# Optimization experiments

Hardware: AMD Instinct MI355X
Metric: run time of the kernel (lower is better)

## Reference

```python
import jax, jax.numpy as jnp
import numpy as np
import math

N_HEADS = 8
TANH_CLIP = 10.0
TEMP = 1.0


def setup_inputs() -> dict:
    key = jax.random.key(0)
    ks = jax.random.split(key, 8)
    B, N, D = 256, 2048, 128
    node_embeddings = jax.random.normal(ks[0], (B, N, D), dtype=jnp.float32)
    W_node = jax.random.normal(ks[1], (D, 3 * D), dtype=jnp.float32) / math.sqrt(D)
    W_fixed = jax.random.normal(ks[2], (D, D), dtype=jnp.float32) / math.sqrt(D)
    W_step = jax.random.normal(ks[3], (2 * D, D), dtype=jnp.float32) / math.sqrt(2 * D)
    W_out = jax.random.normal(ks[4], (D, D), dtype=jnp.float32) / math.sqrt(D)
    first_idx = jax.random.randint(ks[5], (B,), 0, N, dtype=jnp.int32)
    last_idx = jax.random.randint(ks[6], (B,), 0, N, dtype=jnp.int32)
    mask = jax.random.bernoulli(ks[7], 0.5, (B, N))
    mask = mask.at[:, 0].set(False)  # guarantee at least one feasible node per row
    return {"node_embeddings": node_embeddings, "W_node": W_node, "W_fixed": W_fixed,
            "W_step": W_step, "W_out": W_out, "first_idx": first_idx,
            "last_idx": last_idx, "mask": mask}


def reference(node_embeddings, W_node, W_fixed, W_step, W_out, first_idx, last_idx, mask):
    B, N, D = node_embeddings.shape
    H = N_HEADS
    hd = D // H  # key_dim = val_dim = embed_dim / n_heads
    neg_inf = -jnp.inf

    # --- _precompute ---
    graph_embed = node_embeddings.mean(axis=1)                # [B, D]
    fixed_context = graph_embed @ W_fixed                     # [B, D]
    proj = node_embeddings @ W_node                           # [B, N, 3D]
    gK, gV, logit_K = jnp.split(proj, 3, axis=-1)             # each [B, N, D]
    gK = gK.reshape(B, N, H, hd).transpose(2, 0, 1, 3)        # [H, B, N, hd]
    gV = gV.reshape(B, N, H, hd).transpose(2, 0, 1, 3)        # [H, B, N, hd]

    # --- step context: cat(first node emb, last node emb) ---
    first_emb = jnp.take_along_axis(node_embeddings, first_idx[:, None, None].astype(jnp.int32), axis=1)[:, 0]  # [B, D]
    last_emb = jnp.take_along_axis(node_embeddings, last_idx[:, None, None].astype(jnp.int32), axis=1)[:, 0]
    step_ctx = jnp.concatenate([first_emb, last_emb], axis=-1)  # [B, 2D]
    query = fixed_context + step_ctx @ W_step                 # [B, D]

    # --- glimpse multi-head attention (n_query = 1, masked inner) ---
    Q = query.reshape(B, H, hd).transpose(1, 0, 2)            # [H, B, hd]
    compat = jnp.einsum('hbd,hbnd->hbn', Q, gK) / math.sqrt(hd)  # [H, B, N]
    compat = jnp.where(mask[None, :, :], neg_inf, compat)     # mask_inner=True
    attn = jax.nn.softmax(compat, axis=-1)
    heads = jnp.einsum('hbn,hbnd->hbd', attn, gV)             # [H, B, hd]
    glimpse = heads.transpose(1, 0, 2).reshape(B, D) @ W_out  # project_out, [B, D]

    # --- logits with tanh clipping and masking ---
    logits = jnp.einsum('bd,bnd->bn', glimpse, logit_K) / math.sqrt(D)  # [B, N]
    logits = jnp.tanh(logits) * TANH_CLIP
    logits = jnp.where(mask, neg_inf, logits)                 # mask_logits=True
    log_p = jax.nn.log_softmax(logits / TEMP, axis=-1)        # [B, N]
    return log_p
```

## Files before the change

### kernel.cpp

```cpp
#include <hip/hip_runtime.h>
#include <math.h>

#define B_ 256
#define N_ 2048
#define D_ 128

#define NEG_HUGE (-1.0e30f)

#define WSA_STRIDE 1040
#define WSA_SIZE (B_ * 8 * WSA_STRIDE)
#define WSB_OFF WSA_SIZE
#define WSB_SIZE (B_ * 8 * 2)
#define WSC_OFF (WSB_OFF + WSB_SIZE)
#define WSC_SIZE (B_ * D_)
#define WS_FLOATS (WSC_OFF + WSC_SIZE)

__device__ __forceinline__ float wave_max64(float v) {
#pragma unroll
  for (int off = 32; off > 0; off >>= 1) v = fmaxf(v, __shfl_xor(v, off, 64));
  return v;
}
__device__ __forceinline__ float wave_sum64(float v) {
#pragma unroll
  for (int off = 32; off > 0; off >>= 1) v += __shfl_xor(v, off, 64);
  return v;
}

__global__ void __launch_bounds__(128) k_partial(const float* __restrict__ emb,
                                                 float* __restrict__ buf) {
  const int b = blockIdx.x, s = blockIdx.y;
  const int t = threadIdx.x;
  const int f4 = t & 31, ng = t >> 5;
  const float4* base = (const float4*)(emb + (size_t)b * N_ * D_);
  float4 acc = make_float4(0.f, 0.f, 0.f, 0.f);
  int n = s * 256 + ng;
#pragma unroll 4
  for (int i = 0; i < 64; ++i, n += 4) {
    float4 v = base[(size_t)n * 32 + f4];
    acc.x += v.x; acc.y += v.y; acc.z += v.z; acc.w += v.w;
  }
  __shared__ float4 red[128];
  red[t] = acc;
  __syncthreads();
  if (ng == 0) {
    float4 a = red[f4], bb = red[32 + f4], c = red[64 + f4], d = red[96 + f4];
    float4 r = make_float4(a.x + bb.x + c.x + d.x, a.y + bb.y + c.y + d.y,
                           a.z + bb.z + c.z + d.z, a.w + bb.w + c.w + d.w);
    *((float4*)(buf + (size_t)b * N_ + s * 128) + f4) = r;
  }
}

__global__ void __launch_bounds__(128) k_query(const float* __restrict__ emb,
                                               const float* __restrict__ Wfix,
                                               const float* __restrict__ Wstep,
                                               const float* __restrict__ Wnode,
                                               const int* __restrict__ fidx,
                                               const int* __restrict__ lidx,
                                               float* __restrict__ buf) {
  const int b = blockIdx.x, t = threadIdx.x;
  __shared__ float ge[128], fe[128], le[128], q[128];
  float s = 0.f;
  const float* part = buf + (size_t)b * N_;
#pragma unroll
  for (int i = 0; i < 8; ++i) s += part[i * 128 + t];
  ge[t] = s * (1.0f / 2048.0f);
  const int fi = fidx[b], li = lidx[b];
  fe[t] = emb[(size_t)b * N_ * D_ + (size_t)fi * D_ + t];
  le[t] = emb[(size_t)b * N_ * D_ + (size_t)li * D_ + t];
  __syncthreads();
  float acc = 0.f;
  for (int k = 0; k < 128; ++k) acc = fmaf(ge[k], Wfix[k * 128 + t], acc);
  for (int k = 0; k < 128; ++k) acc = fmaf(fe[k], Wstep[k * 128 + t], acc);
  for (int k = 0; k < 128; ++k) acc = fmaf(le[k], Wstep[(128 + k) * 128 + t], acc);
  q[t] = acc;
  __syncthreads();
  const float* wrow = Wnode + (size_t)t * 384;
#pragma unroll
  for (int h = 0; h < 8; ++h) {
    float a = 0.f;
#pragma unroll
    for (int k = 0; k < 16; ++k) a = fmaf(q[h * 16 + k], wrow[h * 16 + k], a);
    buf[(size_t)b * N_ + 1024 + h * 128 + t] = a * 0.25f;
  }
}

__global__ void __launch_bounds__(256) k_attn_part(const float* __restrict__ emb,
                                                   const unsigned char* __restrict__ mask,
                                                   const float* __restrict__ buf,
                                                   float* __restrict__ wsA) {
  const int b = blockIdx.x, s = blockIdx.y;
  const int t = threadIdx.x;
  const int lane = t & 63;
  const int hb = t >> 6;
  const int h0 = hb, h1 = hb + 4;

  __shared__ __align__(16) float emb_lds[64][132];
  __shared__ __align__(16) float qh_s[8 * 128];
  __shared__ unsigned char mask_s[64];

  {
    const float* src = buf + (size_t)b * N_ + 1024;
    for (int i = t; i < 1024; i += 256) qh_s[i] = src[i];
  }

  float m0 = -INFINITY, m1 = -INFINITY, l0 = 0.f, l1 = 0.f;
  float w00 = 0.f, w01 = 0.f, w10 = 0.f, w11 = 0.f;
  const int d0 = lane, d1 = lane + 64;
  const float* embb = emb + (size_t)b * N_ * D_;
  const unsigned char* mrow = mask + (size_t)b * N_;

  __syncthreads();

  for (int tile = 0; tile < 4; ++tile) {
    const int n0 = s * 256 + tile * 64;
    {
      int gid = t;
#pragma unroll
      for (int i = 0; i < 8; ++i, gid += 256) {
        int r = gid >> 5, c4 = gid & 31;
        float4 v = *(const float4*)(embb + (size_t)(n0 + r) * D_ + c4 * 4);
        *(float4*)&emb_lds[r][c4 * 4] = v;
      }
      if (t < 64) mask_s[t] = mrow[n0 + t];
    }
    __syncthreads();

    float s0 = 0.f, s1 = 0.f;
    {
      const float* er = &emb_lds[lane][0];
      const float* q0r = &qh_s[h0 * 128];
      const float* q1r = &qh_s[h1 * 128];
#pragma unroll 8
      for (int k = 0; k < 32; ++k) {
        float4 e = *(const float4*)(er + 4 * k);
        float4 qa = *(const float4*)(q0r + 4 * k);
        float4 qb = *(const float4*)(q1r + 4 * k);
        s0 = fmaf(e.x, qa.x, fmaf(e.y, qa.y, fmaf(e.z, qa.z, fmaf(e.w, qa.w, s0))));
        s1 = fmaf(e.x, qb.x, fmaf(e.y, qb.y, fmaf(e.z, qb.z, fmaf(e.w, qb.w, s1))));
      }
    }
    const bool msk = mask_s[lane] != 0;
    if (msk) { s0 = -INFINITY; s1 = -INFINITY; }

    const float tm0 = wave_max64(s0), tm1 = wave_max64(s1);
    const float mn0 = fmaxf(m0, tm0), mn1 = fmaxf(m1, tm1);
    const float r0 = (mn0 == -INFINITY) ? 1.f : expf(m0 - mn0);
    const float r1 = (mn1 == -INFINITY) ? 1.f : expf(m1 - mn1);
    const float p0 = msk ? 0.f : expf(s0 - mn0);
    const float p1 = msk ? 0.f : expf(s1 - mn1);
    l0 = l0 * r0 + wave_sum64(p0);
    l1 = l1 * r1 + wave_sum64(p1);
    m0 = mn0; m1 = mn1;

    w00 *= r0; w01 *= r0; w10 *= r1; w11 *= r1;
#pragma unroll 4
    for (int n = 0; n < 64; ++n) {
      const float pa = __int_as_float(__builtin_amdgcn_readlane(__float_as_int(p0), n));
      const float pb = __int_as_float(__builtin_amdgcn_readlane(__float_as_int(p1), n));
      const float e0 = emb_lds[n][d0];
      const float e1 = emb_lds[n][d1];
      w00 = fmaf(pa, e0, w00); w01 = fmaf(pa, e1, w01);
      w10 = fmaf(pb, e0, w10); w11 = fmaf(pb, e1, w11);
    }
    __syncthreads();
  }

  float* dst = wsA + (size_t)(b * 8 + s) * WSA_STRIDE;
  dst[16 + h0 * 128 + d0] = w00;
  dst[16 + h0 * 128 + d1] = w01;
  dst[16 + h1 * 128 + d0] = w10;
  dst[16 + h1 * 128 + d1] = w11;
  if (lane == 0) {
    dst[h0] = m0; dst[8 + h0] = l0;
    dst[h1] = m1; dst[8 + h1] = l1;
  }
}

__global__ void __launch_bounds__(128) k_attn_comb(const float* __restrict__ Wnode,
                                                   const float* __restrict__ Wout,
                                                   const float* __restrict__ wsA,
                                                   float* __restrict__ wsC) {
  const int b = blockIdx.x, t = threadIdx.x;
  const float* base = wsA + (size_t)b * 8 * WSA_STRIDE;
  __shared__ float Ls[8], scale[8][8];
  __shared__ float wl[8 * 128], heads[128], glim[128];

  if (t < 8) {
    float M = -INFINITY;
#pragma unroll
    for (int s = 0; s < 8; ++s) M = fmaxf(M, base[s * WSA_STRIDE + t]);
    float L = 0.f;
#pragma unroll
    for (int s = 0; s < 8; ++s) {
      const float m = base[s * WSA_STRIDE + t];
      const float sc = (m == -INFINITY) ? 0.f : expf(m - M);
      scale[s][t] = sc;
      L = fmaf(base[s * WSA_STRIDE + 8 + t], sc, L);
    }
    Ls[t] = L;
  }
  __syncthreads();

#pragma unroll
  for (int h = 0; h < 8; ++h) {
    float acc = 0.f;
#pragma unroll
    for (int s = 0; s < 8; ++s)
      acc = fmaf(scale[s][h], base[s * WSA_STRIDE + 16 + h * 128 + t], acc);
    wl[h * 128 + t] = acc;
  }
  __syncthreads();

  {
    const int h = t >> 4, k = t & 15;
    float hv = 0.f;
    const float* wp = Wnode + 128 + h * 16 + k;
    for (int d = 0; d < 128; ++d) hv = fmaf(wl[h * 128 + d], wp[(size_t)d * 384], hv);
    heads[t] = hv / Ls[h];
  }
  __syncthreads();
  {
    float g = 0.f;
    for (int j = 0; j < 128; ++j) g = fmaf(heads[j], Wout[j * 128 + t], g);
    glim[t] = g;
  }
  __syncthreads();
  {
    float cv = 0.f;
    const float* wr = Wnode + (size_t)t * 384 + 256;
    for (int j = 0; j < 128; ++j) cv = fmaf(wr[j], glim[j], cv);
    wsC[(size_t)b * 128 + t] = cv * 0.08838834764831845f;
  }
}

__global__ void __launch_bounds__(256) k_logits_part(const float* __restrict__ emb,
                                                     const unsigned char* __restrict__ mask,
                                                     const float* __restrict__ wsC,
                                                     float* __restrict__ buf,
                                                     float* __restrict__ wsB) {
  const int b = blockIdx.x, s = blockIdx.y;
  const int t = threadIdx.x, lane = t & 63, w = t >> 6;
  __shared__ __align__(16) float emb_lds[64][132];
  __shared__ float part[4][64];
  const float* embb = emb + (size_t)b * N_ * D_;
  const unsigned char* mrow = mask + (size_t)b * N_;

  float4 cq[8];
  {
    const float4* c4 = (const float4*)(wsC + (size_t)b * 128);
#pragma unroll
    for (int j = 0; j < 8; ++j) cq[j] = c4[w * 8 + j];
  }

  float mr = NEG_HUGE, sr = 0.f;
  for (int tile = 0; tile < 4; ++tile) {
    const int n0 = s * 256 + tile * 64;
    {
      int gid = t;
#pragma unroll
      for (int i = 0; i < 8; ++i, gid += 256) {
        int r = gid >> 5, c4i = gid & 31;
        *(float4*)&emb_lds[r][c4i * 4] =
            *(const float4*)(embb + (size_t)(n0 + r) * D_ + c4i * 4);
      }
    }
    __syncthreads();

    const float* er = &emb_lds[lane][w * 32];
    float acc = 0.f;
#pragma unroll
    for (int j = 0; j < 8; ++j) {
      float4 e = *(const float4*)(er + 4 * j);
      acc = fmaf(e.x, cq[j].x, fmaf(e.y, cq[j].y, fmaf(e.z, cq[j].z, fmaf(e.w, cq[j].w, acc))));
    }
    part[w][lane] = acc;
    __syncthreads();

    const float v = part[0][lane] + part[1][lane] + part[2][lane] + part[3][lane];
    const bool msk = mrow[n0 + lane] != 0;
    const float val = msk ? NEG_HUGE : 10.f * tanhf(v);
    const float tm = wave_max64(val);
    const float mn = fmaxf(mr, tm);
    sr = sr * expf(mr - mn) + wave_sum64(msk ? 0.f : expf(val - mn));
    mr = mn;
    if (w == 0) buf[(size_t)b * N_ + n0 + lane] = val;
    __syncthreads();
  }
  if (t == 0) {
    wsB[(size_t)(b * 8 + s) * 2] = mr;
    wsB[(size_t)(b * 8 + s) * 2 + 1] = sr;
  }
}

__global__ void __launch_bounds__(256) k_norm(const float* __restrict__ wsB,
                                              float* __restrict__ buf) {
  const int b = blockIdx.x, t = threadIdx.x;
  __shared__ float LSs;
  if (t == 0) {
    float M = NEG_HUGE;
#pragma unroll
    for (int s = 0; s < 8; ++s) M = fmaxf(M, wsB[(size_t)(b * 8 + s) * 2]);
    float S = 0.f;
#pragma unroll
    for (int s = 0; s < 8; ++s) {
      const float m = wsB[(size_t)(b * 8 + s) * 2];
      S += wsB[(size_t)(b * 8 + s) * 2 + 1] * expf(m - M);
    }
    LSs = M + logf(S);
  }
  __syncthreads();
  const float LS = LSs;
#pragma unroll
  for (int i = 0; i < 8; ++i) {
    const size_t idx = (size_t)b * N_ + t + 256 * i;
    const float v = buf[idx];
    buf[idx] = (v <= -1.0e29f) ? NEG_HUGE : (v - LS);
  }
}

__global__ void __launch_bounds__(256) k_attn(const float* __restrict__ emb,
                                              const float* __restrict__ Wnode,
                                              const float* __restrict__ Wout,
                                              const unsigned char* __restrict__ mask,
                                              float* __restrict__ buf) {
  const int b = blockIdx.x;
  const int t = threadIdx.x;
  const int lane = t & 63;
  const int hb = t >> 6;
  const int h0 = hb, h1 = hb + 4;

  __shared__ __align__(16) float emb_lds[64][132];
  __shared__ __align__(16) float qh_s[8 * 128];
  __shared__ float heads_lds[128];
  __shared__ float glim_lds[128];
  __shared__ float l_lds[8];
  __shared__ unsigned char mask_s[64];

  {
    const float* src = buf + (size_t)b * N_ + 1024;
    for (int i = t; i < 1024; i += 256) qh_s[i] = src[i];
  }
  float m0 = -INFINITY, m1 = -INFINITY, l0 = 0.f, l1 = 0.f;
  float w00 = 0.f, w01 = 0.f, w10 = 0.f, w11 = 0.f;
  const int d0 = lane, d1 = lane + 64;
  const float* embb = emb + (size_t)b * N_ * D_;
  const unsigned char* mrow = mask + (size_t)b * N_;
  __syncthreads();
  for (int tile = 0; tile < N_ / 64; ++tile) {
    const int n0 = tile * 64;
    int gid = t;
#pragma unroll
    for (int i = 0; i < 8; ++i, gid += 256) {
      int r = gid >> 5, c4 = gid & 31;
      *(float4*)&emb_lds[r][c4 * 4] = *(const float4*)(embb + (size_t)(n0 + r) * D_ + c4 * 4);
    }
    if (t < 64) mask_s[t] = mrow[n0 + t];
    __syncthreads();
    float s0 = 0.f, s1 = 0.f;
    const float* er = &emb_lds[lane][0];
    const float* q0r = &qh_s[h0 * 128];
    const float* q1r = &qh_s[h1 * 128];
#pragma unroll 8
    for (int k = 0; k < 32; ++k) {
      float4 e = *(const float4*)(er + 4 * k);
      float4 qa = *(const float4*)(q0r + 4 * k);
      float4 qb = *(const float4*)(q1r + 4 * k);
      s0 = fmaf(e.x, qa.x, fmaf(e.y, qa.y, fmaf(e.z, qa.z, fmaf(e.w, qa.w, s0))));
      s1 = fmaf(e.x, qb.x, fmaf(e.y, qb.y, fmaf(e.z, qb.z, fmaf(e.w, qb.w, s1))));
    }
    const bool msk = mask_s[lane] != 0;
    if (msk) { s0 = -INFINITY; s1 = -INFINITY; }
    const float tm0 = wave_max64(s0), tm1 = wave_max64(s1);
    const float mn0 = fmaxf(m0, tm0), mn1 = fmaxf(m1, tm1);
    const float r0 = (mn0 == -INFINITY) ? 1.f : expf(m0 - mn0);
    const float r1 = (mn1 == -INFINITY) ? 1.f : expf(m1 - mn1);
    const float p0 = msk ? 0.f : expf(s0 - mn0);
    const float p1 = msk ? 0.f : expf(s1 - mn1);
    l0 = l0 * r0 + wave_sum64(p0);
    l1 = l1 * r1 + wave_sum64(p1);
    m0 = mn0; m1 = mn1;
    w00 *= r0; w01 *= r0; w10 *= r1; w11 *= r1;
#pragma unroll 4
    for (int n = 0; n < 64; ++n) {
      const float pa = __int_as_float(__builtin_amdgcn_readlane(__float_as_int(p0), n));
      const float pb = __int_as_float(__builtin_amdgcn_readlane(__float_as_int(p1), n));
      const float e0 = emb_lds[n][d0];
      const float e1 = emb_lds[n][d1];
      w00 = fmaf(pa, e0, w00); w01 = fmaf(pa, e1, w01);
      w10 = fmaf(pb, e0, w10); w11 = fmaf(pb, e1, w11);
    }
    __syncthreads();
  }
  float* wl = &emb_lds[0][0];
  wl[h0 * 128 + d0] = w00; wl[h0 * 128 + d1] = w01;
  wl[h1 * 128 + d0] = w10; wl[h1 * 128 + d1] = w11;
  if (lane == 0) { l_lds[h0] = l0; l_lds[h1] = l1; }
  __syncthreads();
  if (t < 128) {
    const int h = t >> 4, k = t & 15;
    float hv = 0.f;
    const float* wp = Wnode + 128 + h * 16 + k;
    for (int d = 0; d < 128; ++d) hv = fmaf(wl[h * 128 + d], wp[(size_t)d * 384], hv);
    heads_lds[h * 16 + k] = hv / l_lds[h];
  }
  __syncthreads();
  if (t < 128) {
    float g = 0.f;
    for (int j = 0; j < 128; ++j) g = fmaf(heads_lds[j], Wout[j * 128 + t], g);
    glim_lds[t] = g;
  }
  __syncthreads();
  if (t < 128) {
    float cv = 0.f;
    const float* wr = Wnode + (size_t)t * 384 + 256;
    for (int j = 0; j < 128; ++j) cv = fmaf(wr[j], glim_lds[j], cv);
    buf[(size_t)b * N_ + t] = cv * 0.08838834764831845f;
  }
}

__global__ void __launch_bounds__(256) k_logits(const float* __restrict__ emb,
                                                const unsigned char* __restrict__ mask,
                                                float* __restrict__ buf) {
  const int b = blockIdx.x, t = threadIdx.x;
  const int lane = t & 63, w = t >> 6;
  __shared__ float lg[N_];
  __shared__ float redmax[4], redsum[4];
  const float c0 = buf[(size_t)b * N_ + 2 * lane];
  const float c1 = buf[(size_t)b * N_ + 2 * lane + 1];
  const float2* ebase = (const float2*)(emb + (size_t)b * N_ * D_);
  for (int i = 0; i < 64; ++i) {
    const int n0 = w * 512 + i * 8;
    float sarr[8];
#pragma unroll
    for (int j = 0; j < 8; ++j) {
      float2 e = ebase[(size_t)(n0 + j) * 64 + lane];
      sarr[j] = fmaf(e.x, c0, e.y * c1);
    }
#pragma unroll
    for (int j = 0; j < 8; ++j) {
      const float v = wave_sum64(sarr[j]);
      if (lane == j) lg[n0 + j] = v;
    }
  }
  __syncthreads();
  const unsigned char* mrow = mask + (size_t)b * N_;
  float v[8];
  float vmax = NEG_HUGE;
#pragma unroll
  for (int i = 0; i < 8; ++i) {
    const int n = t + 256 * i;
    const float val = mrow[n] ? NEG_HUGE : 10.f * tanhf(lg[n]);
    v[i] = val;
    vmax = fmaxf(vmax, val);
  }
  vmax = wave_max64(vmax);
  if (lane == 0) redmax[w] = vmax;
  __syncthreads();
  const float M = fmaxf(fmaxf(redmax[0], redmax[1]), fmaxf(redmax[2], redmax[3]));
  float ss = 0.f;
#pragma unroll
  for (int i = 0; i < 8; ++i) ss += expf(v[i] - M);
  ss = wave_sum64(ss);
  if (lane == 0) redsum[w] = ss;
  __syncthreads();
  const float S = redsum[0] + redsum[1] + redsum[2] + redsum[3];
  const float LS = M + logf(S);
#pragma unroll
  for (int i = 0; i < 8; ++i) {
    const int n = t + 256 * i;
    buf[(size_t)b * N_ + n] = mrow[n] ? NEG_HUGE : (v[i] - LS);
  }
}

extern "C" void kernel_launch(void* const* d_in, const int* in_sizes, int n_in,
                              void* d_out, int out_size, void* d_ws, size_t ws_size,
                              hipStream_t stream) {
  (void)in_sizes; (void)n_in; (void)out_size;
  const float* emb = (const float*)d_in[0];
  const float* Wnode = (const float*)d_in[1];
  const float* Wfix = (const float*)d_in[2];
  const float* Wstep = (const float*)d_in[3];
  const float* Wout = (const float*)d_in[4];
  const int* fidx = (const int*)d_in[5];
  const int* lidx = (const int*)d_in[6];
  const unsigned char* mask = (const unsigned char*)d_in[7];
  float* buf = (float*)d_out;

  k_partial<<<dim3(B_, 8), 128, 0, stream>>>(emb, buf);
  k_query<<<B_, 128, 0, stream>>>(emb, Wfix, Wstep, Wnode, fidx, lidx, buf);

  if (ws_size >= (size_t)WS_FLOATS * sizeof(float)) {
    float* ws = (float*)d_ws;
    k_attn_part<<<dim3(B_, 8), 256, 0, stream>>>(emb, mask, buf, ws);
    k_attn_comb<<<B_, 128, 0, stream>>>(Wnode, Wout, ws, ws + WSC_OFF);
    k_logits_part<<<dim3(B_, 8), 256, 0, stream>>>(emb, mask, ws + WSC_OFF, buf, ws + WSB_OFF);
    k_norm<<<B_, 256, 0, stream>>>(ws + WSB_OFF, buf);
  } else {
    k_attn<<<B_, 256, 0, stream>>>(emb, Wnode, Wout, mask, buf);
    k_logits<<<B_, 256, 0, stream>>>(emb, mask, buf);
  }
}
```

Before: 199.8 us.

## Stage embeddings as bf16 copy and fuse query and combine into attention/logit kernels

A new prep kernel reads the fp32 embeddings once. It computes the per-slice mean partials and writes a bf16 (round-to-nearest-even) copy of the embeddings into workspace. The attention and logit kernels then stream this half-size copy instead of the fp32 tensor. The query projection is folded into the attention-partial kernel and the head combine/projection into the logit-partial kernel, cutting the launch count from six to four. In exchange, the small matvecs are recomputed redundantly in each of the 8 slice blocks, the path needs a large workspace, and the bf16 keys and values add numerical error.

```diff
diff --git a/kernel.cpp b/kernel.cpp
--- a/kernel.cpp
+++ b/kernel.cpp
@@ -7,13 +7,20 @@
 
 #define NEG_HUGE (-1.0e30f)
 
+#define WSE_USHORTS ((size_t)B_ * N_ * D_)
+#define WSE_BYTES (WSE_USHORTS * 2)
+#define WSM_FLOATS (B_ * 8 * 128)
 #define WSA_STRIDE 1040
-#define WSA_SIZE (B_ * 8 * WSA_STRIDE)
-#define WSB_OFF WSA_SIZE
-#define WSB_SIZE (B_ * 8 * 2)
-#define WSC_OFF (WSB_OFF + WSB_SIZE)
-#define WSC_SIZE (B_ * D_)
-#define WS_FLOATS (WSC_OFF + WSC_SIZE)
+#define WSA_FLOATS (B_ * 8 * WSA_STRIDE)
+#define WSB_FLOATS (B_ * 8 * 2)
+#define WS_NEW_BYTES (WSE_BYTES + (size_t)(WSM_FLOATS + WSA_FLOATS + WSB_FLOATS) * 4)
+
+#define OLD_WSA_SIZE (B_ * 8 * WSA_STRIDE)
+#define OLD_WSB_OFF OLD_WSA_SIZE
+#define OLD_WSB_SIZE (B_ * 8 * 2)
+#define OLD_WSC_OFF (OLD_WSB_OFF + OLD_WSB_SIZE)
+#define OLD_WSC_SIZE (B_ * D_)
+#define OLD_WS_FLOATS (OLD_WSC_OFF + OLD_WSC_SIZE)
 
 __device__ __forceinline__ float wave_max64(float v) {
 #pragma unroll
@@ -26,68 +33,63 @@
   return v;
 }
 
-__global__ void __launch_bounds__(128) k_partial(const float* __restrict__ emb,
-                                                 float* __restrict__ buf) {
-  const int b = blockIdx.x, s = blockIdx.y;
-  const int t = threadIdx.x;
-  const int f4 = t & 31, ng = t >> 5;
-  const float4* base = (const float4*)(emb + (size_t)b * N_ * D_);
+__device__ __forceinline__ unsigned short bf16rne(float f) {
+  unsigned u = __float_as_uint(f);
+  u += 0x7FFFu + ((u >> 16) & 1u);
+  return (unsigned short)(u >> 16);
+}
+__device__ __forceinline__ void unpack8(uint4 u, float* dst) {
+  dst[0] = __uint_as_float(u.x << 16);
+  dst[1] = __uint_as_float(u.x & 0xFFFF0000u);
+  dst[2] = __uint_as_float(u.y << 16);
+  dst[3] = __uint_as_float(u.y & 0xFFFF0000u);
+  dst[4] = __uint_as_float(u.z << 16);
+  dst[5] = __uint_as_float(u.z & 0xFFFF0000u);
+  dst[6] = __uint_as_float(u.w << 16);
+  dst[7] = __uint_as_float(u.w & 0xFFFF0000u);
+}
+
+
+__global__ void __launch_bounds__(256) k_prep(const float* __restrict__ emb,
+                                              unsigned short* __restrict__ wsE,
+                                              float* __restrict__ wsM) {
+  const int b = blockIdx.x, s = blockIdx.y, t = threadIdx.x;
+  const int f4 = t & 31, g = t >> 5;
+  const size_t rowbase = (size_t)b * N_;
   float4 acc = make_float4(0.f, 0.f, 0.f, 0.f);
-  int n = s * 256 + ng;
+  int n = s * 256 + g;
 #pragma unroll 4
-  for (int i = 0; i < 64; ++i, n += 4) {
-    float4 v = base[(size_t)n * 32 + f4];
+  for (int i = 0; i < 32; ++i, n += 8) {
+    const float4 v = *(const float4*)(emb + (rowbase + n) * D_ + f4 * 4);
     acc.x += v.x; acc.y += v.y; acc.z += v.z; acc.w += v.w;
-  }
-  __shared__ float4 red[128];
+    ushort4 o;
+    o.x = bf16rne(v.x); o.y = bf16rne(v.y); o.z = bf16rne(v.z); o.w = bf16rne(v.w);
+    *(ushort4*)(wsE + (rowbase + n) * D_ + f4 * 4) = o;
+  }
+  __shared__ float4 red[256];
   red[t] = acc;
   __syncthreads();
-  if (ng == 0) {
-    float4 a = red[f4], bb = red[32 + f4], c = red[64 + f4], d = red[96 + f4];
-    float4 r = make_float4(a.x + bb.x + c.x + d.x, a.y + bb.y + c.y + d.y,
-                           a.z + bb.z + c.z + d.z, a.w + bb.w + c.w + d.w);
-    *((float4*)(buf + (size_t)b * N_ + s * 128) + f4) = r;
-  }
-}
-
-__global__ void __launch_bounds__(128) k_query(const float* __restrict__ emb,
+  if (g == 0) {
+    float4 r = red[f4];
+#pragma unroll
+    for (int j = 1; j < 8; ++j) {
+      const float4 a = red[j * 32 + f4];
+      r.x += a.x; r.y += a.y; r.z += a.z; r.w += a.w;
+    }
+    *(float4*)(wsM + (size_t)(b * 8 + s) * 128 + f4 * 4) = r;
+  }
+}
+
+__global__ void __launch_bounds__(256) k_attn2(const float* __restrict__ emb,
+                                               const unsigned short* __restrict__ wsE,
+                                               const float* __restrict__ wsM,
                                                const float* __restrict__ Wfix,
                                                const float* __restrict__ Wstep,
                                                const float* __restrict__ Wnode,
                                                const int* __restrict__ fidx,
                                                const int* __restrict__ lidx,
-                                               float* __restrict__ buf) {
-  const int b = blockIdx.x, t = threadIdx.x;
-  __shared__ float ge[128], fe[128], le[128], q[128];
-  float s = 0.f;
-  const float* part = buf + (size_t)b * N_;
-#pragma unroll
-  for (int i = 0; i < 8; ++i) s += part[i * 128 + t];
-  ge[t] = s * (1.0f / 2048.0f);
-  const int fi = fidx[b], li = lidx[b];
-  fe[t] = emb[(size_t)b * N_ * D_ + (size_t)fi * D_ + t];
-  le[t] = emb[(size_t)b * N_ * D_ + (size_t)li * D_ + t];
-  __syncthreads();
-  float acc = 0.f;
-  for (int k = 0; k < 128; ++k) acc = fmaf(ge[k], Wfix[k * 128 + t], acc);
-  for (int k = 0; k < 128; ++k) acc = fmaf(fe[k], Wstep[k * 128 + t], acc);
-  for (int k = 0; k < 128; ++k) acc = fmaf(le[k], Wstep[(128 + k) * 128 + t], acc);
-  q[t] = acc;
-  __syncthreads();
-  const float* wrow = Wnode + (size_t)t * 384;
-#pragma unroll
-  for (int h = 0; h < 8; ++h) {
-    float a = 0.f;
-#pragma unroll
-    for (int k = 0; k < 16; ++k) a = fmaf(q[h * 16 + k], wrow[h * 16 + k], a);
-    buf[(size_t)b * N_ + 1024 + h * 128 + t] = a * 0.25f;
-  }
-}
-
-__global__ void __launch_bounds__(256) k_attn_part(const float* __restrict__ emb,
-                                                   const unsigned char* __restrict__ mask,
-                                                   const float* __restrict__ buf,
-                                                   float* __restrict__ wsA) {
+                                               const unsigned char* __restrict__ mask,
+                                               float* __restrict__ wsA) {
   const int b = blockIdx.x, s = blockIdx.y;
   const int t = threadIdx.x;
   const int lane = t & 63;
@@ -96,17 +98,41 @@
 
   __shared__ __align__(16) float emb_lds[64][132];
   __shared__ __align__(16) float qh_s[8 * 128];
+  __shared__ float ge[128], fe[128], le[128], q_s[128];
   __shared__ unsigned char mask_s[64];
 
-  {
-    const float* src = buf + (size_t)b * N_ + 1024;
-    for (int i = t; i < 1024; i += 256) qh_s[i] = src[i];
+  if (t < 128) {
+    float ssum = 0.f;
+#pragma unroll
+    for (int i = 0; i < 8; ++i) ssum += wsM[(size_t)(b * 8 + i) * 128 + t];
+    ge[t] = ssum * (1.0f / 2048.0f);
+    fe[t] = emb[((size_t)b * N_ + fidx[b]) * D_ + t];
+    le[t] = emb[((size_t)b * N_ + lidx[b]) * D_ + t];
+  }
+  __syncthreads();
+  if (t < 128) {
+    float acc = 0.f;
+    for (int k = 0; k < 128; ++k) acc = fmaf(ge[k], Wfix[k * 128 + t], acc);
+    for (int k = 0; k < 128; ++k) acc = fmaf(fe[k], Wstep[k * 128 + t], acc);
+    for (int k = 0; k < 128; ++k) acc = fmaf(le[k], Wstep[(128 + k) * 128 + t], acc);
+    q_s[t] = acc;
+  }
+  __syncthreads();
+  if (t < 128) {
+    const float* wrow = Wnode + (size_t)t * 384;
+#pragma unroll
+    for (int h = 0; h < 8; ++h) {
+      float a = 0.f;
+#pragma unroll
+      for (int k = 0; k < 16; ++k) a = fmaf(q_s[h * 16 + k], wrow[h * 16 + k], a);
+      qh_s[h * 128 + t] = a * 0.25f;
+    }
   }
 
   float m0 = -INFINITY, m1 = -INFINITY, l0 = 0.f, l1 = 0.f;
   float w00 = 0.f, w01 = 0.f, w10 = 0.f, w11 = 0.f;
   const int d0 = lane, d1 = lane + 64;
-  const float* embb = emb + (size_t)b * N_ * D_;
+  const unsigned short* embE = wsE + (size_t)b * N_ * D_;
   const unsigned char* mrow = mask + (size_t)b * N_;
 
   __syncthreads();
@@ -114,12 +140,16 @@
   for (int tile = 0; tile < 4; ++tile) {
     const int n0 = s * 256 + tile * 64;
     {
+      const unsigned short* src = embE + (size_t)n0 * D_;
       int gid = t;
 #pragma unroll
-      for (int i = 0; i < 8; ++i, gid += 256) {
-        int r = gid >> 5, c4 = gid & 31;
-        float4 v = *(const float4*)(embb + (size_t)(n0 + r) * D_ + c4 * 4);
-        *(float4*)&emb_lds[r][c4 * 4] = v;
+      for (int i = 0; i < 4; ++i, gid += 256) {
+        const int r = gid >> 4, c8 = (gid & 15) * 8;
+        const uint4 u = *(const uint4*)(src + (size_t)r * D_ + c8);
+        float f[8];
+        unpack8(u, f);
+        *(float4*)&emb_lds[r][c8] = make_float4(f[0], f[1], f[2], f[3]);
+        *(float4*)&emb_lds[r][c8 + 4] = make_float4(f[4], f[5], f[6], f[7]);
       }
       if (t < 64) mask_s[t] = mrow[n0 + t];
     }
@@ -176,42 +206,49 @@
   }
 }
 
-__global__ void __launch_bounds__(128) k_attn_comb(const float* __restrict__ Wnode,
-                                                   const float* __restrict__ Wout,
-                                                   const float* __restrict__ wsA,
-                                                   float* __restrict__ wsC) {
-  const int b = blockIdx.x, t = threadIdx.x;
+__global__ void __launch_bounds__(256) k_logits2(const unsigned short* __restrict__ wsE,
+                                                 const unsigned char* __restrict__ mask,
+                                                 const float* __restrict__ Wnode,
+                                                 const float* __restrict__ Wout,
+                                                 const float* __restrict__ wsA,
+                                                 float* __restrict__ buf,
+                                                 float* __restrict__ wsB) {
+  const int b = blockIdx.x, s = blockIdx.y;
+  const int t = threadIdx.x, lane = t & 63, w = t >> 6;
+  __shared__ __align__(16) float emb_lds[64][132];
+  __shared__ float heads[128], glim[128], c_s[128];
+  __shared__ float Ls[8], scale_s[8][8];
+  __shared__ float part[4][64];
+
   const float* base = wsA + (size_t)b * 8 * WSA_STRIDE;
-  __shared__ float Ls[8], scale[8][8];
-  __shared__ float wl[8 * 128], heads[128], glim[128];
-
   if (t < 8) {
     float M = -INFINITY;
 #pragma unroll
-    for (int s = 0; s < 8; ++s) M = fmaxf(M, base[s * WSA_STRIDE + t]);
+    for (int q = 0; q < 8; ++q) M = fmaxf(M, base[q * WSA_STRIDE + t]);
     float L = 0.f;
 #pragma unroll
-    for (int s = 0; s < 8; ++s) {
-      const float m = base[s * WSA_STRIDE + t];
+    for (int q = 0; q < 8; ++q) {
+      const float m = base[q * WSA_STRIDE + t];
       const float sc = (m == -INFINITY) ? 0.f : expf(m - M);
-      scale[s][t] = sc;
-      L = fmaf(base[s * WSA_STRIDE + 8 + t], sc, L);
+      scale_s[q][t] = sc;
+      L = fmaf(base[q * WSA_STRIDE + 8 + t], sc, L);
     }
     Ls[t] = L;
   }
   __syncthreads();
-
-#pragma unroll
-  for (int h = 0; h < 8; ++h) {
-    float acc = 0.f;
-#pragma unroll
-    for (int s = 0; s < 8; ++s)
-      acc = fmaf(scale[s][h], base[s * WSA_STRIDE + 16 + h * 128 + t], acc);
-    wl[h * 128 + t] = acc;
-  }
-  __syncthreads();
-
-  {
+  float* wl = &emb_lds[0][0];
+  if (t < 128) {
+#pragma unroll
+    for (int h = 0; h < 8; ++h) {
+      float acc = 0.f;
+#pragma unroll
+      for (int q = 0; q < 8; ++q)
+        acc = fmaf(scale_s[q][h], base[q * WSA_STRIDE + 16 + h * 128 + t], acc);
+      wl[h * 128 + t] = acc;
+    }
+  }
+  __syncthreads();
+  if (t < 128) {
     const int h = t >> 4, k = t & 15;
     float hv = 0.f;
     const float* wp = Wnode + 128 + h * 16 + k;
@@ -219,49 +256,44 @@
     heads[t] = hv / Ls[h];
   }
   __syncthreads();
-  {
+  if (t < 128) {
     float g = 0.f;
     for (int j = 0; j < 128; ++j) g = fmaf(heads[j], Wout[j * 128 + t], g);
     glim[t] = g;
   }
   __syncthreads();
-  {
+  if (t < 128) {
     float cv = 0.f;
     const float* wr = Wnode + (size_t)t * 384 + 256;
     for (int j = 0; j < 128; ++j) cv = fmaf(wr[j], glim[j], cv);
-    wsC[(size_t)b * 128 + t] = cv * 0.08838834764831845f;
-  }
-}
-
-__global__ void __launch_bounds__(256) k_logits_part(const float* __restrict__ emb,
-                                                     const unsigned char* __restrict__ mask,
-                                                     const float* __restrict__ wsC,
-                                                     float* __restrict__ buf,
-                                                     float* __restrict__ wsB) {
-  const int b = blockIdx.x, s = blockIdx.y;
-  const int t = threadIdx.x, lane = t & 63, w = t >> 6;
-  __shared__ __align__(16) float emb_lds[64][132];
-  __shared__ float part[4][64];
-  const float* embb = emb + (size_t)b * N_ * D_;
-  const unsigned char* mrow = mask + (size_t)b * N_;
+    c_s[t] = cv * 0.08838834764831845f;
+  }
+  __syncthreads();
 
   float4 cq[8];
   {
-    const float4* c4 = (const float4*)(wsC + (size_t)b * 128);
+    const float4* c4 = (const float4*)c_s;
 #pragma unroll
     for (int j = 0; j < 8; ++j) cq[j] = c4[w * 8 + j];
   }
-
+  __syncthreads();
+
+  const unsigned short* embE = wsE + (size_t)b * N_ * D_;
+  const unsigned char* mrow = mask + (size_t)b * N_;
   float mr = NEG_HUGE, sr = 0.f;
   for (int tile = 0; tile < 4; ++tile) {
     const int n0 = s * 256 + tile * 64;
     {
+      const unsigned short* src = embE + (size_t)n0 * D_;
       int gid = t;
 #pragma unroll
-      for (int i = 0; i < 8; ++i, gid += 256) {
-        int r = gid >> 5, c4i = gid & 31;
-        *(float4*)&emb_lds[r][c4i * 4] =
-            *(const float4*)(embb + (size_t)(n0 + r) * D_ + c4i * 4);
+      for (int i = 0; i < 4; ++i, gid += 256) {
+        const int r = gid >> 4, c8 = (gid & 15) * 8;
+        const uint4 u = *(const uint4*)(src + (size_t)r * D_ + c8);
+        float f[8];
+        unpack8(u, f);
+        *(float4*)&emb_lds[r][c8] = make_float4(f[0], f[1], f[2], f[3]);
+        *(float4*)&emb_lds[r][c8 + 4] = make_float4(f[4], f[5], f[6], f[7]);
       }
     }
     __syncthreads();
@@ -299,12 +331,12 @@
   if (t == 0) {
     float M = NEG_HUGE;
 #pragma unroll
-    for (int s = 0; s < 8; ++s) M = fmaxf(M, wsB[(size_t)(b * 8 + s) * 2]);
+    for (int q = 0; q < 8; ++q) M = fmaxf(M, wsB[(size_t)(b * 8 + q) * 2]);
     float S = 0.f;
 #pragma unroll
-    for (int s = 0; s < 8; ++s) {
-      const float m = wsB[(size_t)(b * 8 + s) * 2];
-      S += wsB[(size_t)(b * 8 + s) * 2 + 1] * expf(m - M);
+    for (int q = 0; q < 8; ++q) {
+      const float m = wsB[(size_t)(b * 8 + q) * 2];
+      S += wsB[(size_t)(b * 8 + q) * 2 + 1] * expf(m - M);
     }
     LSs = M + logf(S);
   }
@@ -318,12 +350,70 @@
   }
 }
 
-__global__ void __launch_bounds__(256) k_attn(const float* __restrict__ emb,
-                                              const float* __restrict__ Wnode,
-                                              const float* __restrict__ Wout,
-                                              const unsigned char* __restrict__ mask,
-                                              float* __restrict__ buf) {
-  const int b = blockIdx.x;
+
+__global__ void __launch_bounds__(128) k_partial(const float* __restrict__ emb,
+                                                 float* __restrict__ buf) {
+  const int b = blockIdx.x, s = blockIdx.y;
+  const int t = threadIdx.x;
+  const int f4 = t & 31, ng = t >> 5;
+  const float4* base = (const float4*)(emb + (size_t)b * N_ * D_);
+  float4 acc = make_float4(0.f, 0.f, 0.f, 0.f);
+  int n = s * 256 + ng;
+#pragma unroll 4
+  for (int i = 0; i < 64; ++i, n += 4) {
+    float4 v = base[(size_t)n * 32 + f4];
+    acc.x += v.x; acc.y += v.y; acc.z += v.z; acc.w += v.w;
+  }
+  __shared__ float4 red[128];
+  red[t] = acc;
+  __syncthreads();
+  if (ng == 0) {
+    float4 a = red[f4], bb = red[32 + f4], c = red[64 + f4], d = red[96 + f4];
+    float4 r = make_float4(a.x + bb.x + c.x + d.x, a.y + bb.y + c.y + d.y,
+                           a.z + bb.z + c.z + d.z, a.w + bb.w + c.w + d.w);
+    *((float4*)(buf + (size_t)b * N_ + s * 128) + f4) = r;
+  }
+}
+
+__global__ void __launch_bounds__(128) k_query(const float* __restrict__ emb,
+                                               const float* __restrict__ Wfix,
+                                               const float* __restrict__ Wstep,
+                                               const float* __restrict__ Wnode,
+                                               const int* __restrict__ fidx,
+                                               const int* __restrict__ lidx,
+                                               float* __restrict__ buf) {
+  const int b = blockIdx.x, t = threadIdx.x;
+  __shared__ float ge[128], fe[128], le[128], q[128];
+  float s = 0.f;
+  const float* part = buf + (size_t)b * N_;
+#pragma unroll
+  for (int i = 0; i < 8; ++i) s += part[i * 128 + t];
+  ge[t] = s * (1.0f / 2048.0f);
+  const int fi = fidx[b], li = lidx[b];
+  fe[t] = emb[(size_t)b * N_ * D_ + (size_t)fi * D_ + t];
+  le[t] = emb[(size_t)b * N_ * D_ + (size_t)li * D_ + t];
+  __syncthreads();
+  float acc = 0.f;
+  for (int k = 0; k < 128; ++k) acc = fmaf(ge[k], Wfix[k * 128 + t], acc);
+  for (int k = 0; k < 128; ++k) acc = fmaf(fe[k], Wstep[k * 128 + t], acc);
+  for (int k = 0; k < 128; ++k) acc = fmaf(le[k], Wstep[(128 + k) * 128 + t], acc);
+  q[t] = acc;
+  __syncthreads();
+  const float* wrow = Wnode + (size_t)t * 384;
+#pragma unroll
+  for (int h = 0; h < 8; ++h) {
+    float a = 0.f;
+#pragma unroll
+    for (int k = 0; k < 16; ++k) a = fmaf(q[h * 16 + k], wrow[h * 16 + k], a);
+    buf[(size_t)b * N_ + 1024 + h * 128 + t] = a * 0.25f;
+  }
+}
+
+__global__ void __launch_bounds__(256) k_attn_part(const float* __restrict__ emb,
+                                                   const unsigned char* __restrict__ mask,
+                                                   const float* __restrict__ buf,
+                                                   float* __restrict__ wsA) {
+  const int b = blockIdx.x, s = blockIdx.y;
   const int t = threadIdx.x;
   const int lane = t & 63;
   const int hb = t >> 6;
@@ -331,9 +421,6 @@
 
   __shared__ __align__(16) float emb_lds[64][132];
   __shared__ __align__(16) float qh_s[8 * 128];
-  __shared__ float heads_lds[128];
-  __shared__ float glim_lds[128];
-  __shared__ float l_lds[8];
   __shared__ unsigned char mask_s[64];
 
   {
@@ -346,8 +433,8 @@
   const float* embb = emb + (size_t)b * N_ * D_;
   const unsigned char* mrow = mask + (size_t)b * N_;
   __syncthreads();
-  for (int tile = 0; tile < N_ / 64; ++tile) {
-    const int n0 = tile * 64;
+  for (int tile = 0; tile < 4; ++tile) {
+    const int n0 = s * 256 + tile * 64;
     int gid = t;
 #pragma unroll
     for (int i = 0; i < 8; ++i, gid += 256) {
@@ -391,84 +478,123 @@
     }
     __syncthreads();
   }
-  float* wl = &emb_lds[0][0];
-  wl[h0 * 128 + d0] = w00; wl[h0 * 128 + d1] = w01;
-  wl[h1 * 128 + d0] = w10; wl[h1 * 128 + d1] = w11;
-  if (lane == 0) { l_lds[h0] = l0; l_lds[h1] = l1; }
-  __syncthreads();
-  if (t < 128) {
+  float* dst = wsA + (size_t)(b * 8 + s) * WSA_STRIDE;
+  dst[16 + h0 * 128 + d0] = w00;
+  dst[16 + h0 * 128 + d1] = w01;
+  dst[16 + h1 * 128 + d0] = w10;
+  dst[16 + h1 * 128 + d1] = w11;
+  if (lane == 0) {
+    dst[h0] = m0; dst[8 + h0] = l0;
+    dst[h1] = m1; dst[8 + h1] = l1;
+  }
+}
+
+__global__ void __launch_bounds__(128) k_attn_comb(const float* __restrict__ Wnode,
+                                                   const float* __restrict__ Wout,
+                                                   const float* __restrict__ wsA,
+                                                   float* __restrict__ wsC) {
+  const int b = blockIdx.x, t = threadIdx.x;
+  const float* base = wsA + (size_t)b * 8 * WSA_STRIDE;
+  __shared__ float Ls[8], scale[8][8];
+  __shared__ float wl[8 * 128], heads[128], glim[128];
+
+  if (t < 8) {
+    float M = -INFINITY;
+#pragma unroll
+    for (int s = 0; s < 8; ++s) M = fmaxf(M, base[s * WSA_STRIDE + t]);
+    float L = 0.f;
+#pragma unroll
+    for (int s = 0; s < 8; ++s) {
+      const float m = base[s * WSA_STRIDE + t];
+      const float sc = (m == -INFINITY) ? 0.f : expf(m - M);
+      scale[s][t] = sc;
+      L = fmaf(base[s * WSA_STRIDE + 8 + t], sc, L);
+    }
+    Ls[t] = L;
+  }
+  __syncthreads();
+#pragma unroll
+  for (int h = 0; h < 8; ++h) {
+    float acc = 0.f;
+#pragma unroll
+    for (int s = 0; s < 8; ++s)
+      acc = fmaf(scale[s][h], base[s * WSA_STRIDE + 16 + h * 128 + t], acc);
+    wl[h * 128 + t] = acc;
+  }
+  __syncthreads();
+  {
     const int h = t >> 4, k = t & 15;
     float hv = 0.f;
     const float* wp = Wnode + 128 + h * 16 + k;
     for (int d = 0; d < 128; ++d) hv = fmaf(wl[h * 128 + d], wp[(size_t)d * 384], hv);
-    heads_lds[h * 16 + k] = hv / l_lds[h];
-  }
-  __syncthreads();
-  if (t < 128) {
+    heads[t] = hv / Ls[h];
+  }
+  __syncthreads();
+  {
     float g = 0.f;
-    for (int j = 0; j < 128; ++j) g = fmaf(heads_lds[j], Wout[j * 128 + t], g);
-    glim_lds[t] = g;
-  }
-  __syncthreads();
-  if (t < 128) {
+    for (int j = 0; j < 128; ++j) g = fmaf(heads[j], Wout[j * 128 + t], g);
+    glim[t] = g;
+  }
+  __syncthreads();
+  {
     float cv = 0.f;
     const float* wr = Wnode + (size_t)t * 384 + 256;
-    for (int j = 0; j < 128; ++j) cv = fmaf(wr[j], glim_lds[j], cv);
-    buf[(size_t)b * N_ + t] = cv * 0.08838834764831845f;
-  }
-}
-
-__global__ void __launch_bounds__(256) k_logits(const float* __restrict__ emb,
-                                                const unsigned char* __restrict__ mask,
-                                                float* __restrict__ buf) {
-  const int b = blockIdx.x, t = threadIdx.x;
-  const int lane = t & 63, w = t >> 6;
-  __shared__ float lg[N_];
-  __shared__ float redmax[4], redsum[4];
-  const float c0 = buf[(size_t)b * N_ + 2 * lane];
-  const float c1 = buf[(size_t)b * N_ + 2 * lane + 1];
-  const float2* ebase = (const float2*)(emb + (size_t)b * N_ * D_);
-  for (int i = 0; i < 64; ++i) {
-    const int n0 = w * 512 + i * 8;
-    float sarr[8];
+    for (int j = 0; j < 128; ++j) cv = fmaf(wr[j], glim[j], cv);
+    wsC[(size_t)b * 128 + t] = cv * 0.08838834764831845f;
+  }
+}
+
+__global__ void __launch_bounds__(256) k_logits_part(const float* __restrict__ emb,
+                                                     const unsigned char* __restrict__ mask,
+                                                     const float* __restrict__ wsC,
+                                                     float* __restrict__ buf,
+                                                     float* __restrict__ wsB) {
+  const int b = blockIdx.x, s = blockIdx.y;
+  const int t = threadIdx.x, lane = t & 63, w = t >> 6;
+  __shared__ __align__(16) float emb_lds[64][132];
+  __shared__ float part[4][64];
+  const float* embb = emb + (size_t)b * N_ * D_;
+  const unsigned char* mrow = mask + (size_t)b * N_;
+
+  float4 cq[8];
+  {
+    const float4* c4 = (const float4*)(wsC + (size_t)b * 128);
+#pragma unroll
+    for (int j = 0; j < 8; ++j) cq[j] = c4[w * 8 + j];
+  }
+  float mr = NEG_HUGE, sr = 0.f;
+  for (int tile = 0; tile < 4; ++tile) {
+    const int n0 = s * 256 + tile * 64;
+    int gid = t;
+#pragma unroll
+    for (int i = 0; i < 8; ++i, gid += 256) {
+      int r = gid >> 5, c4i = gid & 31;
+      *(float4*)&emb_lds[r][c4i * 4] =
+          *(const float4*)(embb + (size_t)(n0 + r) * D_ + c4i * 4);
+    }
+    __syncthreads();
+    const float* er = &emb_lds[lane][w * 32];
+    float acc = 0.f;
 #pragma unroll
     for (int j = 0; j < 8; ++j) {
-      float2 e = ebase[(size_t)(n0 + j) * 64 + lane];
-      sarr[j] = fmaf(e.x, c0, e.y * c1);
-    }
-#pragma unroll
-    for (int j = 0; j < 8; ++j) {
-      const float v = wave_sum64(sarr[j]);
-      if (lane == j) lg[n0 + j] = v;
-    }
-  }
-  __syncthreads();
-  const unsigned char* mrow = mask + (size_t)b * N_;
-  float v[8];
-  float vmax = NEG_HUGE;
-#pragma unroll
-  for (int i = 0; i < 8; ++i) {
-    const int n = t + 256 * i;
-    const float val = mrow[n] ? NEG_HUGE : 10.f * tanhf(lg[n]);
-    v[i] = val;
-    vmax = fmaxf(vmax, val);
-  }
-  vmax = wave_max64(vmax);
-  if (lane == 0) redmax[w] = vmax;
-  __syncthreads();
-  const float M = fmaxf(fmaxf(redmax[0], redmax[1]), fmaxf(redmax[2], redmax[3]));
-  float ss = 0.f;
-#pragma unroll
-  for (int i = 0; i < 8; ++i) ss += expf(v[i] - M);
-  ss = wave_sum64(ss);
-  if (lane == 0) redsum[w] = ss;
-  __syncthreads();
-  const float S = redsum[0] + redsum[1] + redsum[2] + redsum[3];
-  const float LS = M + logf(S);
-#pragma unroll
-  for (int i = 0; i < 8; ++i) {
-    const int n = t + 256 * i;
-    buf[(size_t)b * N_ + n] = mrow[n] ? NEG_HUGE : (v[i] - LS);
+      float4 e = *(const float4*)(er + 4 * j);
+      acc = fmaf(e.x, cq[j].x, fmaf(e.y, cq[j].y, fmaf(e.z, cq[j].z, fmaf(e.w, cq[j].w, acc))));
+    }
+    part[w][lane] = acc;
+    __syncthreads();
+    const float v = part[0][lane] + part[1][lane] + part[2][lane] + part[3][lane];
+    const bool msk = mrow[n0 + lane] != 0;
+    const float val = msk ? NEG_HUGE : 10.f * tanhf(v);
+    const float tm = wave_max64(val);
+    const float mn = fmaxf(mr, tm);
+    sr = sr * expf(mr - mn) + wave_sum64(msk ? 0.f : expf(val - mn));
+    mr = mn;
+    if (w == 0) buf[(size_t)b * N_ + n0 + lane] = val;
+    __syncthreads();
+  }
+  if (t == 0) {
+    wsB[(size_t)(b * 8 + s) * 2] = mr;
+    wsB[(size_t)(b * 8 + s) * 2 + 1] = sr;
   }
 }
 
@@ -486,17 +612,25 @@
   const unsigned char* mask = (const unsigned char*)d_in[7];
   float* buf = (float*)d_out;
 
-  k_partial<<<dim3(B_, 8), 128, 0, stream>>>(emb, buf);
-  k_query<<<B_, 128, 0, stream>>>(emb, Wfix, Wstep, Wnode, fidx, lidx, buf);
-
-  if (ws_size >= (size_t)WS_FLOATS * sizeof(float)) {
+  if (ws_size >= WS_NEW_BYTES) {
+    unsigned short* wsE = (unsigned short*)d_ws;
+    float* fbase = (float*)d_ws + WSE_USHORTS / 2;
+    float* wsM = fbase;
+    float* wsA = fbase + WSM_FLOATS;
+    float* wsB = wsA + WSA_FLOATS;
+    k_prep<<<dim3(B_, 8), 256, 0, stream>>>(emb, wsE, wsM);
+    k_attn2<<<dim3(B_, 8), 256, 0, stream>>>(emb, wsE, wsM, Wfix, Wstep, Wnode,
+                                             fidx, lidx, mask, wsA);
+    k_logits2<<<dim3(B_, 8), 256, 0, stream>>>(wsE, mask, Wnode, Wout, wsA, buf, wsB);
+    k_norm<<<B_, 256, 0, stream>>>(wsB, buf);
+  } else {
     float* ws = (float*)d_ws;
+    k_partial<<<dim3(B_, 8), 128, 0, stream>>>(emb, buf);
+    k_query<<<B_, 128, 0, stream>>>(emb, Wfix, Wstep, Wnode, fidx, lidx, buf);
     k_attn_part<<<dim3(B_, 8), 256, 0, stream>>>(emb, mask, buf, ws);
-    k_attn_comb<<<B_, 128, 0, stream>>>(Wnode, Wout, ws, ws + WSC_OFF);
-    k_logits_part<<<dim3(B_, 8), 256, 0, stream>>>(emb, mask, ws + WSC_OFF, buf, ws + WSB_OFF);
-    k_norm<<<B_, 256, 0, stream>>>(ws + WSB_OFF, buf);
-  } else {
-    k_attn<<<B_, 256, 0, stream>>>(emb, Wnode, Wout, mask, buf);
-    k_logits<<<B_, 256, 0, stream>>>(emb, mask, buf);
-  }
-}
+    k_attn_comb<<<B_, 128, 0, stream>>>(Wnode, Wout, ws, ws + OLD_WSC_OFF);
+    k_logits_part<<<dim3(B_, 8), 256, 0, stream>>>(emb, mask, ws + OLD_WSC_OFF, buf,
+                                                   ws + OLD_WSB_OFF);
+    k_norm<<<B_, 256, 0, stream>>>(ws + OLD_WSB_OFF, buf);
+  }
+}
```

Result: slower. 238.6 us (+19.5%).
